# Performance work log

Hardware: AMD Instinct MI355X
Metric: run time of the kernel (lower is better)

## Reference

```python
import jax, jax.numpy as jnp
import numpy as np

B, C, H, W = 4, 256, 224, 224
WH = WW = 8
SH = SW = 4
HEADS = 8
HD = C // HEADS
N = WH * WW
EPS = 1e-5


def _rel_index():
    coords = np.stack(np.meshgrid(np.arange(WH), np.arange(WW), indexing='ij')).reshape(2, -1)
    rel = (coords[:, :, None] - coords[:, None, :]).transpose(1, 2, 0).copy()
    rel[:, :, 0] += WH - 1
    rel[:, :, 1] += WW - 1
    rel[:, :, 0] *= 2 * WW - 1
    return rel.sum(-1)  # (N, N) int

REL_INDEX = _rel_index()


def _shift_mask(Hp, Wp):
    # Swin shift mask for one image: (nW, N, N) float, 0 or -100
    img = np.zeros((Hp, Wp))
    cnt = 0
    for a, b in [(0, Hp - WH), (Hp - WH, Hp - SH), (Hp - SH, Hp)]:
        for c, d in [(0, Wp - WW), (Wp - WW, Wp - SW), (Wp - SW, Wp)]:
            img[a:b, c:d] = cnt
            cnt += 1
    mw = img.reshape(Hp // WH, WH, Wp // WW, WW).transpose(0, 2, 1, 3).reshape(-1, N)
    diff = mw[:, None, :] - mw[:, :, None]  # [w, i, j] = mw[w,j] - mw[w,i]
    return np.where(diff != 0, np.float32(-100.0), np.float32(0.0)).astype(np.float32)


def _ln(x, w, b):
    m = jnp.mean(x, axis=-1, keepdims=True)
    v = jnp.mean(jnp.square(x - m), axis=-1, keepdims=True)
    return (x - m) * jax.lax.rsqrt(v + EPS) * w + b


def setup_inputs() -> dict:
    key = jax.random.key(0)
    ks = jax.random.split(key, 8)
    num_rel = (2 * WH - 1) * (2 * WW - 1)
    return {
        'x': jax.random.normal(ks[0], (B, C, H, W), dtype=jnp.float32),
        'qkv_w': jax.random.normal(ks[1], (3 * C, C), dtype=jnp.float32) * 0.02,
        'proj_w': jax.random.normal(ks[2], (C, C), dtype=jnp.float32) * 0.02,
        'proj_b': jnp.zeros((C,), dtype=jnp.float32),
        'rpb_table': jax.random.normal(ks[3], (num_rel, HEADS), dtype=jnp.float32) * 0.02,
        'norm1_w': jnp.ones((C,), dtype=jnp.float32),
        'norm1_b': jnp.zeros((C,), dtype=jnp.float32),
        'norm2_w': jnp.ones((C,), dtype=jnp.float32),
        'norm2_b': jnp.zeros((C,), dtype=jnp.float32),
        'mlp_w1': jax.random.normal(ks[4], (4 * C, C), dtype=jnp.float32) * 0.02,
        'mlp_b1': jnp.zeros((4 * C,), dtype=jnp.float32),
        'mlp_w2': jax.random.normal(ks[5], (C, 4 * C), dtype=jnp.float32) * 0.02,
        'mlp_b2': jnp.zeros((C,), dtype=jnp.float32),
    }


def reference(x, qkv_w, proj_w, proj_b, rpb_table, norm1_w, norm1_b,
              norm2_w, norm2_b, mlp_w1, mlp_b1, mlp_w2, mlp_b2):
    Bx, Cx, Hx, Wx = x.shape
    pad_h = (WH - Hx % WH) % WH
    pad_w = (WW - Wx % WW) % WW
    if pad_h or pad_w:
        x = jnp.pad(x, ((0, 0), (0, 0), (0, pad_h), (0, pad_w)))
    Hp, Wp = Hx + pad_h, Wx + pad_w
    x = jnp.transpose(x, (0, 2, 3, 1))                    # BHWC
    x = jnp.roll(x, (-SH, -SW), axis=(1, 2))
    nW = (Hp // WH) * (Wp // WW)
    # window partition -> (B*nW, N, C), batch-major
    xw = x.reshape(Bx, Hp // WH, WH, Wp // WW, WW, Cx)
    xw = jnp.transpose(xw, (0, 1, 3, 2, 4, 5)).reshape(-1, N, Cx)

    # ----- windowed attention -----
    h = _ln(xw, norm1_w, norm1_b)
    qkv = (h @ qkv_w.T).reshape(-1, N, 3, HEADS, HD)
    qkv = jnp.transpose(qkv, (2, 0, 3, 1, 4))             # (3, Bw, heads, N, hd)
    q, k, v = qkv[0], qkv[1], qkv[2]
    attn = jnp.einsum('bhnd,bhmd->bhnm', q, k) * (1.0 / HD ** 0.5)
    bias = jnp.transpose(rpb_table[REL_INDEX.reshape(-1)].reshape(N, N, HEADS), (2, 0, 1))
    attn = attn + bias[None]
    # faithful to torch: repeat_interleave(B, dim=0) -> window-major mask ordering
    mask = jnp.asarray(_shift_mask(Hp, Wp))               # (nW, N, N)
    attn = attn + jnp.repeat(mask, Bx, axis=0)[:, None]
    attn = jax.nn.softmax(attn, axis=-1)
    out = jnp.einsum('bhnm,bhmd->bhnd', attn, v)
    out = jnp.transpose(out, (0, 2, 1, 3)).reshape(-1, N, Cx)
    out = out @ proj_w.T + proj_b
    xw = xw + out

    # ----- MLP -----
    h = _ln(xw, norm2_w, norm2_b)
    h = jax.nn.gelu(h @ mlp_w1.T + mlp_b1, approximate=False) @ mlp_w2.T + mlp_b2
    xw = xw + h

    # window reverse, un-shift, un-pad
    x = xw.reshape(Bx, Hp // WH, Wp // WW, WH, WW, Cx)
    x = jnp.transpose(x, (0, 1, 3, 2, 4, 5)).reshape(Bx, Hp, Wp, Cx)
    x = jnp.roll(x, (SH, SW), axis=(1, 2))
    x = x[:, :Hx, :Wx, :]
    return jnp.transpose(x, (0, 3, 1, 2))
```

## Files before the change

### kernel.cpp

```cpp
#include <hip/hip_runtime.h>

typedef unsigned short u16;
typedef unsigned int   u32;
typedef __attribute__((ext_vector_type(8))) __bf16 bf16x8;
typedef __attribute__((ext_vector_type(4))) float  f32x4;
typedef __attribute__((ext_vector_type(4))) u16    u16x4;
typedef __attribute__((ext_vector_type(8))) u16    u16x8;

#define DEV __device__ __forceinline__

DEV u16 f2b(float f) {
  union { float f; u32 u; } a; a.f = f;
  const u32 u = a.u;
  return (u16)((u + 0x7fffu + ((u >> 16) & 1u)) >> 16);
}

DEV float gelu_fast(float x) {
  const float x2 = x * x;
  const float t  = __builtin_fmaf(0.1029430f, x2, 2.3022150f);
  const float e  = __builtin_exp2f(x * t);
  const float r  = __builtin_amdgcn_rcpf(1.0f + e);
  return __builtin_fmaf(-x, r, x);
}

DEV void gload16(const void* g, void* l) {
  __builtin_amdgcn_global_load_lds(
      (const __attribute__((address_space(1))) void*)g,
      (__attribute__((address_space(3))) void*)l, 16, 0, 0);
}

__global__ __launch_bounds__(256)
void conv_weights(const float* __restrict__ qkvw, const float* __restrict__ projw,
                  const float* __restrict__ w1,   const float* __restrict__ w2,
                  u16* __restrict__ dq, u16* __restrict__ dp,
                  u16* __restrict__ d1, u16* __restrict__ d2) {
  const int t = blockIdx.x * 256 + threadIdx.x;
  if (t < 196608)      dq[t]          = f2b(qkvw[t]);
  else if (t < 262144) dp[t - 196608] = f2b(projw[t - 196608]);
  else if (t < 524288) d1[t - 262144] = f2b(w1[t - 262144]);
  else                 d2[t - 524288] = f2b(w2[t - 524288]);
}

__global__ __launch_bounds__(256)
void ln1_win(const float* __restrict__ x, const float* __restrict__ w1,
             const float* __restrict__ b1, u16* __restrict__ hout,
             float* __restrict__ xwout) {
  __shared__ float xt[64 * 257];
  __shared__ float smean[256], srstd[256];
  const int tid = threadIdx.x, lane = tid & 63, wv = tid >> 6;
  const int g = blockIdx.x;
  const int b = g / 196, rem = g % 196;
  const int wh = rem / 7, wg = rem % 7;
  const int base_r = b * 784 + wh * 28 + wg * 4;
  const int pr = tid >> 5, pc = tid & 31;
  int hp = wh * 8 + 4 + pr; if (hp >= 224) hp -= 224;
  int wp = wg * 32 + 4 + pc; if (wp >= 224) wp -= 224;
  const long roff = (long)b * 256 * 50176 + hp * 224 + wp;

  float s = 0.f, q = 0.f;
  for (int cc = 0; cc < 4; ++cc) {
#pragma unroll 8
    for (int i = 0; i < 64; ++i) {
      const int c = cc * 64 + i;
      const float v = x[(long)c * 50176 + roff];
      xt[i * 257 + tid] = v;
      s += v; q += v * v;
    }
    __syncthreads();
#pragma unroll 8
    for (int jj = 0; jj < 64; ++jj) {
      const int p = jj * 4 + wv;
      const int m = (base_r + ((p & 31) >> 3)) * 64 + (p >> 5) * 8 + (p & 7);
      xwout[(long)m * 256 + cc * 64 + lane] = xt[lane * 257 + p];
    }
    __syncthreads();
  }
  const float mean = s * (1.f / 256.f);
  smean[tid] = mean;
  srstd[tid] = rsqrtf(q * (1.f / 256.f) - mean * mean + 1e-5f);
  __syncthreads();

  float wr_[4], br_[4];
#pragma unroll
  for (int cc = 0; cc < 4; ++cc) { wr_[cc] = w1[cc * 64 + lane]; br_[cc] = b1[cc * 64 + lane]; }
#pragma unroll 2
  for (int jj = 0; jj < 64; ++jj) {
    const int p = jj * 4 + wv;
    const int m = (base_r + ((p & 31) >> 3)) * 64 + (p >> 5) * 8 + (p & 7);
    const float mu = smean[p], rs = srstd[p];
#pragma unroll
    for (int cc = 0; cc < 4; ++cc) {
      const float v = xwout[(long)m * 256 + cc * 64 + lane];
      hout[(long)m * 256 + cc * 64 + lane] = f2b((v - mu) * rs * wr_[cc] + br_[cc]);
    }
  }
}

template<int EPI, int NCOL>
__global__ __launch_bounds__(1024, 4)
void gemm_bt(const u16* __restrict__ A, const u16* __restrict__ Bw, const int K,
             float* __restrict__ fout, const float* __restrict__ bias,
             u16* __restrict__ bout,
             const float* __restrict__ lnw, const float* __restrict__ lnb,
             float* __restrict__ oout) {
  __shared__ __align__(16) u16 smem[65536];
  u16* sA0 = smem;
  u16* sB0 = smem + 16384;
  u16* sA1 = smem + 32768;
  u16* sB1 = smem + 49152;

  const int tid  = threadIdx.x;
  const int lane = tid & 63;
  const int wid  = tid >> 6;
  const int wrr  = wid >> 2;
  const int wcc  = wid & 3;

  const int nwg = gridDim.x;
  const int bid = blockIdx.x;
  const int wg  = (bid & 7) * (nwg >> 3) + (bid >> 3);
  const int row_blk = wg / NCOL;
  const int col_blk = wg - row_blk * NCOL;
  const int row0 = row_blk * 256;
  const int col0 = col_blk * 256;

  const f32x4 vzero = {0.f, 0.f, 0.f, 0.f};
  f32x4 acc[4][4];
#pragma unroll
  for (int i = 0; i < 4; ++i)
#pragma unroll
    for (int j = 0; j < 4; ++j) acc[i][j] = vzero;

  const int lrow = lane >> 3;
  const int lcol = ((lane & 7) << 3) ^ (lane & 56);
  const int l15  = lane & 15;
  const int l4   = lane >> 4;
  const int ksw  = (lane & 7) << 3;

  const u16* pA = A  + (long)(row0 + wid * 8 + lrow) * K + lcol;
  const u16* pB = Bw + (long)(col0 + wid * 8 + lrow) * K + lcol;

#define STAGE_TILE(KT, DA, DB)                                          \
  {                                                                     \
    _Pragma("unroll")                                                   \
    for (int ch = 0; ch < 2; ++ch) {                                    \
      gload16(pA + (long)(ch * 128) * K + (KT), (DA) + (ch * 128 + wid * 8) * 64); \
      gload16(pB + (long)(ch * 128) * K + (KT), (DB) + (ch * 128 + wid * 8) * 64); \
    }                                                                   \
  }

#define COMPUTE_TILE(SA, SB, SWAP)                                                      \
  {                                                                                     \
    _Pragma("unroll")                                                                   \
    for (int kk = 0; kk < 2; ++kk) {                                                    \
      bf16x8 af[4], bfv[4];                                                             \
      _Pragma("unroll")                                                                 \
      for (int mi = 0; mi < 4; ++mi)                                                    \
        af[mi] = *(const bf16x8*)((SA) + (wrr * 64 + mi * 16 + l15) * 64 +              \
                                  ((kk * 32 + l4 * 8) ^ ksw));                          \
      _Pragma("unroll")                                                                 \
      for (int nj = 0; nj < 4; ++nj)                                                    \
        bfv[nj] = *(const bf16x8*)((SB) + (wcc * 64 + nj * 16 + l15) * 64 +             \
                                   ((kk * 32 + l4 * 8) ^ ksw));                         \
      _Pragma("unroll")                                                                 \
      for (int mi = 0; mi < 4; ++mi)                                                    \
        _Pragma("unroll")                                                               \
        for (int nj = 0; nj < 4; ++nj) {                                                \
          if (SWAP)                                                                     \
            acc[mi][nj] = __builtin_amdgcn_mfma_f32_16x16x32_bf16(bfv[nj], af[mi],      \
                                                                  acc[mi][nj], 0, 0, 0);\
          else                                                                          \
            acc[mi][nj] = __builtin_amdgcn_mfma_f32_16x16x32_bf16(af[mi], bfv[nj],      \
                                                                  acc[mi][nj], 0, 0, 0);\
        }                                                                               \
    }                                                                                   \
  }

#define KLOOP(SWAP)                                                  \
  {                                                                  \
    const int nt = K >> 6;                                           \
    STAGE_TILE(0, sA0, sB0);                                         \
    int cur = 0;                                                     \
    for (int t = 0; t < nt; ++t) {                                   \
      u16* cA = cur ? sA1 : sA0;                                     \
      u16* cB = cur ? sB1 : sB0;                                     \
      u16* nA = cur ? sA0 : sA1;                                     \
      u16* nB = cur ? sB0 : sB1;                                     \
      if (t + 1 < nt) {                                              \
        STAGE_TILE((t + 1) << 6, nA, nB);                            \
        asm volatile("s_waitcnt vmcnt(4)" ::: "memory");             \
      } else {                                                       \
        asm volatile("s_waitcnt vmcnt(0)" ::: "memory");             \
      }                                                              \
      __builtin_amdgcn_s_barrier();                                  \
      asm volatile("" ::: "memory");                                 \
      COMPUTE_TILE(cA, cB, SWAP);                                    \
      asm volatile("" ::: "memory");                                 \
      __builtin_amdgcn_s_barrier();                                  \
      cur ^= 1;                                                      \
    }                                                                \
  }

  if (EPI == 0 && col_blk == 2) {
    KLOOP(0);
#pragma unroll
    for (int mi = 0; mi < 4; ++mi) {
      const int mb = row0 + wrr * 64 + mi * 16 + (l4 << 2);
      const int rrg = mb >> 6, ii = mb & 63;
#pragma unroll
      for (int nj = 0; nj < 4; ++nj) {
        const int n = 512 + wcc * 64 + nj * 16 + l15;
        const int hh = (n >> 5) & 7, d = n & 31;
        u16x4 p;
#pragma unroll
        for (int reg = 0; reg < 4; ++reg) p[reg] = f2b(acc[mi][nj][reg]);
        *(u16x4*)(bout + 102760448L + (long)((rrg * 8 + hh) * 32 + d) * 64 + ii) = p;
      }
    }
    return;
  }

  KLOOP(1);

#undef STAGE_TILE
#undef COMPUTE_TILE
#undef KLOOP

  if (EPI == 0) {
#pragma unroll
    for (int mi = 0; mi < 4; ++mi) {
      const int m = row0 + wrr * 64 + mi * 16 + l15;
      const int rr = m >> 6, ii = m & 63;
#pragma unroll
      for (int nj = 0; nj < 4; ++nj) {
        const int n = col0 + wcc * 64 + nj * 16 + (l4 << 2);
        const int s = n >> 8, hh = (n >> 5) & 7, d = n & 31;
        u16x4 p;
#pragma unroll
        for (int reg = 0; reg < 4; ++reg) p[reg] = f2b(acc[mi][nj][reg]);
        *(u16x4*)(bout + (long)s * 51380224L +
                  (long)((rr * 8 + hh) * 64 + ii) * 32 + d) = p;
      }
    }
  } else if (EPI == 1) {
    f32x4 b4[4];
#pragma unroll
    for (int nj = 0; nj < 4; ++nj)
      b4[nj] = *(const f32x4*)(bias + wcc * 64 + nj * 16 + (l4 << 2));
    float sS[4], sQ[4];
#pragma unroll
    for (int mi = 0; mi < 4; ++mi) {
      const int m = row0 + wrr * 64 + mi * 16 + l15;
      float* yrow = fout + (long)m * 256;
      float s = 0.f, q = 0.f;
#pragma unroll
      for (int nj = 0; nj < 4; ++nj) {
        const int n = wcc * 64 + nj * 16 + (l4 << 2);
        f32x4 o = *(f32x4*)(yrow + n);
#pragma unroll
        for (int reg = 0; reg < 4; ++reg) {
          o[reg] += acc[mi][nj][reg] + b4[nj][reg];
          s += o[reg]; q += o[reg] * o[reg];
        }
        *(f32x4*)(yrow + n) = o;
        acc[mi][nj] = o;
      }
      s += __shfl_xor(s, 16); s += __shfl_xor(s, 32);
      q += __shfl_xor(q, 16); q += __shfl_xor(q, 32);
      sS[mi] = s; sQ[mi] = q;
    }
    float* ps = (float*)smem;
    float* pq = ps + 1024;
    __syncthreads();
    if (lane < 16) {
#pragma unroll
      for (int mi = 0; mi < 4; ++mi) {
        const int idx = ((wrr * 4 + mi) * 16 + l15) * 4 + wcc;
        ps[idx] = sS[mi]; pq[idx] = sQ[mi];
      }
    }
    __syncthreads();
#pragma unroll
    for (int mi = 0; mi < 4; ++mi) {
      const int m = row0 + wrr * 64 + mi * 16 + l15;
      const int base = ((wrr * 4 + mi) * 16 + l15) * 4;
      const float S = ps[base] + ps[base + 1] + ps[base + 2] + ps[base + 3];
      const float Q = pq[base] + pq[base + 1] + pq[base + 2] + pq[base + 3];
      const float mean = S * (1.f / 256.f);
      const float rstd = rsqrtf(Q * (1.f / 256.f) - mean * mean + 1e-5f);
#pragma unroll
      for (int nj = 0; nj < 4; ++nj) {
        const int n = wcc * 64 + nj * 16 + (l4 << 2);
        const f32x4 w4 = *(const f32x4*)(lnw + n);
        const f32x4 c4 = *(const f32x4*)(lnb + n);
        u16x4 p;
#pragma unroll
        for (int reg = 0; reg < 4; ++reg)
          p[reg] = f2b((acc[mi][nj][reg] - mean) * rstd * w4[reg] + c4[reg]);
        *(u16x4*)(bout + (long)m * 256 + n) = p;
      }
    }
  } else if (EPI == 3) {
    f32x4 b4[4];
#pragma unroll
    for (int nj = 0; nj < 4; ++nj)
      b4[nj] = *(const f32x4*)(bias + wcc * 64 + nj * 16 + (l4 << 2));
#pragma unroll
    for (int mi = 0; mi < 4; ++mi) {
      const int m = row0 + wrr * 64 + mi * 16 + l15;
      const float* yrow = fout + (long)m * 256;
#pragma unroll
      for (int nj = 0; nj < 4; ++nj) {
        const int n = wcc * 64 + nj * 16 + (l4 << 2);
        const f32x4 yv = *(const f32x4*)(yrow + n);
#pragma unroll
        for (int reg = 0; reg < 4; ++reg)
          acc[mi][nj][reg] += yv[reg] + b4[nj][reg];
      }
    }
    const int g = row0 >> 8;
    const int b = g / 196, rem = g % 196;
    const int wh = rem / 7, wg2 = rem % 7;
    float* tp = (float*)smem;
    const int pidx = tid & 255, cgrp = tid >> 8;
    const int pr = pidx >> 5, pc = pidx & 31;
    int hp = wh * 8 + 4 + pr; if (hp >= 224) hp -= 224;
    int wp = wg2 * 32 + 4 + pc; if (wp >= 224) wp -= 224;
    float* ob = oout + (long)b * 256 * 50176 + hp * 224 + wp;
    const int pxr = 4 * (pr * 8 + (pc & 7)) + (pc >> 3);
#pragma unroll
    for (int cc = 0; cc < 4; ++cc) {
      __syncthreads();
      if (wcc == cc) {
#pragma unroll
        for (int mi = 0; mi < 4; ++mi) {
          const int pxw = (4 * (mi * 16 + l15) + wrr) ^ l4;
#pragma unroll
          for (int nj = 0; nj < 4; ++nj)
#pragma unroll
            for (int reg = 0; reg < 4; ++reg)
              tp[(nj * 16 + (l4 << 2) + reg) * 256 + pxw] = acc[mi][nj][reg];
        }
      }
      __syncthreads();
#pragma unroll 4
      for (int j = 0; j < 16; ++j) {
        const int c_local = cgrp * 16 + j;
        ob[(long)(cc * 64 + c_local) * 50176] =
            tp[c_local * 256 + (pxr ^ ((j >> 2) & 3))];
      }
    }
  } else if (EPI == 2) {
    f32x4 b4[4];
#pragma unroll
    for (int nj = 0; nj < 4; ++nj)
      b4[nj] = *(const f32x4*)(bias + col0 + wcc * 64 + nj * 16 + (l4 << 2));
#pragma unroll
    for (int mi = 0; mi < 4; ++mi) {
      const int m = row0 + wrr * 64 + mi * 16 + l15;
#pragma unroll
      for (int nj = 0; nj < 4; ++nj) {
        const int n = col0 + wcc * 64 + nj * 16 + (l4 << 2);
        u16x4 p;
#pragma unroll
        for (int reg = 0; reg < 4; ++reg)
          p[reg] = f2b(gelu_fast(acc[mi][nj][reg] + b4[nj][reg]));
        *(u16x4*)(bout + (long)m * 1024 + n) = p;
      }
    }
  }
}

__global__ __launch_bounds__(256)
void attn_win(const u16* __restrict__ qkv, const float* __restrict__ rpb,
              u16* __restrict__ aout) {
  __shared__ u16 Pl[4][4096];
  __shared__ float srpb[1800];
  const int tid = threadIdx.x, lane = tid & 63, wv = tid >> 6;
  const int bid = blockIdx.x;
  const int r = bid >> 1;
  const int h = (bid & 1) * 4 + wv;
  for (int i = tid; i < 1800; i += 256) srpb[i] = rpb[i];
  __syncthreads();

  const int midx = r >> 2;
  const int wh = midx / 28, ww = midx % 28;
  const int l15 = lane & 15, l4 = lane >> 4;

  u16* Pw = &Pl[wv][0];
  const long hb = (long)(r * 8 + h) * 2048;
  const u16* qh = qkv + hb;
  const u16* kh = qkv + 51380224 + hb;
  const u16* vh = qkv + 102760448 + hb;

  int rj[4], cj[4], labj[4];
#pragma unroll
  for (int nj = 0; nj < 4; ++nj) {
    const int j = nj * 16 + l15;
    rj[nj] = j >> 3; cj[nj] = j & 7;
    const int hp = wh * 8 + rj[nj], wp = ww * 8 + cj[nj];
    const int lh = (hp < 216) ? 0 : ((hp < 220) ? 1 : 2);
    const int lw = (wp < 216) ? 0 : ((wp < 220) ? 1 : 2);
    labj[nj] = lh * 3 + lw;
  }

  const f32x4 vzero = {0.f, 0.f, 0.f, 0.f};

  bf16x8 qf[4], kf[4];
#pragma unroll
  for (int mi = 0; mi < 4; ++mi)
    qf[mi] = *(const bf16x8*)(qh + (mi * 16 + l15) * 32 + l4 * 8);
#pragma unroll
  for (int nj = 0; nj < 4; ++nj)
    kf[nj] = *(const bf16x8*)(kh + (nj * 16 + l15) * 32 + l4 * 8);

  f32x4 S[4][4];
#pragma unroll
  for (int mi = 0; mi < 4; ++mi)
#pragma unroll
    for (int nj = 0; nj < 4; ++nj)
      S[mi][nj] = __builtin_amdgcn_mfma_f32_16x16x32_bf16(qf[mi], kf[nj], vzero, 0, 0, 0);

#pragma unroll
  for (int mi = 0; mi < 4; ++mi)
#pragma unroll
    for (int reg = 0; reg < 4; ++reg) {
      const int i = mi * 16 + (l4 << 2) + reg;
      const int ri = i >> 3, ci = i & 7;
      const int hp = wh * 8 + ri, wp = ww * 8 + ci;
      const int lh = (hp < 216) ? 0 : ((hp < 220) ? 1 : 2);
      const int lw = (wp < 216) ? 0 : ((wp < 220) ? 1 : 2);
      const int li = lh * 3 + lw;
      float v[4];
#pragma unroll
      for (int nj = 0; nj < 4; ++nj) {
        const int idx = (ri - rj[nj] + 7) * 15 + (ci - cj[nj] + 7);
        v[nj] = S[mi][nj][reg] * 0.17677669529663687f + srpb[idx * 8 + h]
              + ((li != labj[nj]) ? -100.0f : 0.0f);
      }
      float mx = fmaxf(fmaxf(v[0], v[1]), fmaxf(v[2], v[3]));
      mx = fmaxf(mx, __shfl_xor(mx, 1));
      mx = fmaxf(mx, __shfl_xor(mx, 2));
      mx = fmaxf(mx, __shfl_xor(mx, 4));
      mx = fmaxf(mx, __shfl_xor(mx, 8));
      float sum = 0.f;
#pragma unroll
      for (int nj = 0; nj < 4; ++nj) { v[nj] = __expf(v[nj] - mx); sum += v[nj]; }
      sum += __shfl_xor(sum, 1);
      sum += __shfl_xor(sum, 2);
      sum += __shfl_xor(sum, 4);
      sum += __shfl_xor(sum, 8);
      const float rinv = __builtin_amdgcn_rcpf(sum);
      const int sw = (i & 7) << 3;
#pragma unroll
      for (int nj = 0; nj < 4; ++nj)
        Pw[i * 64 + ((nj * 16 + l15) ^ sw)] = f2b(v[nj] * rinv);
    }

  f32x4 OT[2][4];
#pragma unroll
  for (int td = 0; td < 2; ++td)
#pragma unroll
    for (int ti = 0; ti < 4; ++ti) OT[td][ti] = vzero;

  const int rsw = (l15 & 7) << 3;
#pragma unroll
  for (int kk = 0; kk < 2; ++kk) {
    bf16x8 pf[4], vf[2];
#pragma unroll
    for (int ti = 0; ti < 4; ++ti)
      pf[ti] = *(const bf16x8*)(Pw + (ti * 16 + l15) * 64 + ((kk * 32 + l4 * 8) ^ rsw));
#pragma unroll
    for (int td = 0; td < 2; ++td)
      vf[td] = *(const bf16x8*)(vh + (td * 16 + l15) * 64 + kk * 32 + l4 * 8);
#pragma unroll
    for (int td = 0; td < 2; ++td)
#pragma unroll
      for (int ti = 0; ti < 4; ++ti)
        OT[td][ti] = __builtin_amdgcn_mfma_f32_16x16x32_bf16(vf[td], pf[ti], OT[td][ti], 0, 0, 0);
  }

#pragma unroll
  for (int td = 0; td < 2; ++td)
#pragma unroll
    for (int ti = 0; ti < 4; ++ti) {
      const int i = ti * 16 + l15;
      const int d0 = td * 16 + (l4 << 2);
      u16x4 p;
#pragma unroll
      for (int reg = 0; reg < 4; ++reg) p[reg] = f2b(OT[td][ti][reg]);
      *(u16x4*)(aout + (long)(r * 64 + i) * 256 + h * 32 + d0) = p;
    }
}

extern "C" void kernel_launch(void* const* d_in, const int* in_sizes, int n_in,
                              void* d_out, int out_size, void* d_ws, size_t ws_size,
                              hipStream_t stream) {
  (void)in_sizes; (void)n_in; (void)out_size; (void)ws_size;
  const float* x     = (const float*)d_in[0];
  const float* qkvw  = (const float*)d_in[1];
  const float* projw = (const float*)d_in[2];
  const float* projb = (const float*)d_in[3];
  const float* rpb   = (const float*)d_in[4];
  const float* n1w   = (const float*)d_in[5];
  const float* n1b   = (const float*)d_in[6];
  const float* n2w   = (const float*)d_in[7];
  const float* n2b   = (const float*)d_in[8];
  const float* w1    = (const float*)d_in[9];
  const float* b1    = (const float*)d_in[10];
  const float* w2    = (const float*)d_in[11];
  const float* b2    = (const float*)d_in[12];

  char* ws = (char*)d_ws;
  u16*   hbuf   = (u16*)(ws);
  u16*   qkvb   = (u16*)(ws + 102760448);
  u16*   abuf   = (u16*)(ws + 411041792);
  float* ybuf   = (float*)(ws + 513802240);
  u16*   hidb   = (u16*)(ws + 102760448);
  u16*   qkvwb  = (u16*)(ws + 719323136);
  u16*   projwb = (u16*)(ws + 719716352);
  u16*   w1b    = (u16*)(ws + 719847424);
  u16*   w2b    = (u16*)(ws + 720371712);

  conv_weights<<<3072, 256, 0, stream>>>(qkvw, projw, w1, w2, qkvwb, projwb, w1b, w2b);
  ln1_win<<<784, 256, 0, stream>>>(x, n1w, n1b, hbuf, ybuf);
  gemm_bt<0, 3><<<2352, 1024, 0, stream>>>(hbuf, qkvwb, 256, nullptr, nullptr, qkvb, nullptr, nullptr, nullptr);
  attn_win<<<6272, 256, 0, stream>>>(qkvb, rpb, abuf);
  gemm_bt<1, 1><<<784, 1024, 0, stream>>>(abuf, projwb, 256, ybuf, projb, hbuf, n2w, n2b, nullptr);
  gemm_bt<2, 4><<<3136, 1024, 0, stream>>>(hbuf, w1b, 256, nullptr, b1, hidb, nullptr, nullptr, nullptr);
  gemm_bt<3, 1><<<784, 1024, 0, stream>>>(hidb, w2b, 1024, ybuf, b2, nullptr, nullptr, nullptr, (float*)d_out);
}
```

Baseline: 1.125 ms.

## Shrink GEMM tile to 128x256 with 8 waves and BK=32 staging

Changes the bf16 GEMM from 1024-thread 256x256 tiles with a K-step of 64 to 512-thread 128x256 tiles with a K-step of 32. This cuts LDS use from 128KB to 48KB so more blocks can be resident per CU and the grid doubles. The staging swizzle, LDS fragment loads, LN reduction indexing and the un-window transpose epilogue are rewritten to match. The trade-off is less B-operand reuse per tile and twice as many barriers per K, in exchange for higher occupancy and better load balance.

```diff
diff --git a/kernel.cpp b/kernel.cpp
--- a/kernel.cpp
+++ b/kernel.cpp
@@ -97,17 +97,17 @@
 }
 
 template<int EPI, int NCOL>
-__global__ __launch_bounds__(1024, 4)
+__global__ __launch_bounds__(512, 4)
 void gemm_bt(const u16* __restrict__ A, const u16* __restrict__ Bw, const int K,
              float* __restrict__ fout, const float* __restrict__ bias,
              u16* __restrict__ bout,
              const float* __restrict__ lnw, const float* __restrict__ lnb,
              float* __restrict__ oout) {
-  __shared__ __align__(16) u16 smem[65536];
+  __shared__ __align__(16) u16 smem[24576];
   u16* sA0 = smem;
-  u16* sB0 = smem + 16384;
-  u16* sA1 = smem + 32768;
-  u16* sB1 = smem + 49152;
+  u16* sB0 = smem + 4096;
+  u16* sA1 = smem + 12288;
+  u16* sB1 = smem + 16384;
 
   const int tid  = threadIdx.x;
   const int lane = tid & 63;
@@ -120,7 +120,7 @@
   const int wg  = (bid & 7) * (nwg >> 3) + (bid >> 3);
   const int row_blk = wg / NCOL;
   const int col_blk = wg - row_blk * NCOL;
-  const int row0 = row_blk * 256;
+  const int row0 = row_blk * 128;
   const int col0 = col_blk * 256;
 
   const f32x4 vzero = {0.f, 0.f, 0.f, 0.f};
@@ -130,54 +130,50 @@
 #pragma unroll
     for (int j = 0; j < 4; ++j) acc[i][j] = vzero;
 
-  const int lrow = lane >> 3;
-  const int lcol = ((lane & 7) << 3) ^ (lane & 56);
   const int l15  = lane & 15;
   const int l4   = lane >> 4;
-  const int ksw  = (lane & 7) << 3;
-
-  const u16* pA = A  + (long)(row0 + wid * 8 + lrow) * K + lcol;
-  const u16* pB = Bw + (long)(col0 + wid * 8 + lrow) * K + lcol;
-
-#define STAGE_TILE(KT, DA, DB)                                          \
-  {                                                                     \
-    _Pragma("unroll")                                                   \
-    for (int ch = 0; ch < 2; ++ch) {                                    \
-      gload16(pA + (long)(ch * 128) * K + (KT), (DA) + (ch * 128 + wid * 8) * 64); \
-      gload16(pB + (long)(ch * 128) * K + (KT), (DB) + (ch * 128 + wid * 8) * 64); \
-    }                                                                   \
+  const int ksw2 = (l15 >> 1) & 3;
+  const int lcol = (((tid & 3) ^ ((tid >> 3) & 3)) << 3);
+
+  const u16* pA  = A  + (long)(row0 + (tid >> 2)) * K + lcol;
+  const u16* pB  = Bw + (long)(col0 + (tid >> 2)) * K + lcol;
+  const u16* pB2 = pB + (long)128 * K;
+  const int wbase = wid * 512;
+
+#define STAGE_TILE(KT, DA, DB)                  \
+  {                                             \
+    gload16(pA  + (KT), (DA) + wbase);          \
+    gload16(pB  + (KT), (DB) + wbase);          \
+    gload16(pB2 + (KT), (DB) + 4096 + wbase);   \
   }
 
 #define COMPUTE_TILE(SA, SB, SWAP)                                                      \
   {                                                                                     \
+    bf16x8 af[4], bfv[4];                                                               \
     _Pragma("unroll")                                                                   \
-    for (int kk = 0; kk < 2; ++kk) {                                                    \
-      bf16x8 af[4], bfv[4];                                                             \
+    for (int mi = 0; mi < 4; ++mi)                                                      \
+      af[mi] = *(const bf16x8*)((SA) + (wrr * 64 + mi * 16 + l15) * 32 +                \
+                                ((l4 ^ ksw2) << 3));                                    \
+    _Pragma("unroll")                                                                   \
+    for (int nj = 0; nj < 4; ++nj)                                                      \
+      bfv[nj] = *(const bf16x8*)((SB) + (wcc * 64 + nj * 16 + l15) * 32 +               \
+                                 ((l4 ^ ksw2) << 3));                                   \
+    _Pragma("unroll")                                                                   \
+    for (int mi = 0; mi < 4; ++mi)                                                      \
       _Pragma("unroll")                                                                 \
-      for (int mi = 0; mi < 4; ++mi)                                                    \
-        af[mi] = *(const bf16x8*)((SA) + (wrr * 64 + mi * 16 + l15) * 64 +              \
-                                  ((kk * 32 + l4 * 8) ^ ksw));                          \
-      _Pragma("unroll")                                                                 \
-      for (int nj = 0; nj < 4; ++nj)                                                    \
-        bfv[nj] = *(const bf16x8*)((SB) + (wcc * 64 + nj * 16 + l15) * 64 +             \
-                                   ((kk * 32 + l4 * 8) ^ ksw));                         \
-      _Pragma("unroll")                                                                 \
-      for (int mi = 0; mi < 4; ++mi)                                                    \
-        _Pragma("unroll")                                                               \
-        for (int nj = 0; nj < 4; ++nj) {                                                \
-          if (SWAP)                                                                     \
-            acc[mi][nj] = __builtin_amdgcn_mfma_f32_16x16x32_bf16(bfv[nj], af[mi],      \
-                                                                  acc[mi][nj], 0, 0, 0);\
-          else                                                                          \
-            acc[mi][nj] = __builtin_amdgcn_mfma_f32_16x16x32_bf16(af[mi], bfv[nj],      \
-                                                                  acc[mi][nj], 0, 0, 0);\
-        }                                                                               \
-    }                                                                                   \
+      for (int nj = 0; nj < 4; ++nj) {                                                  \
+        if (SWAP)                                                                       \
+          acc[mi][nj] = __builtin_amdgcn_mfma_f32_16x16x32_bf16(bfv[nj], af[mi],        \
+                                                                acc[mi][nj], 0, 0, 0);  \
+        else                                                                            \
+          acc[mi][nj] = __builtin_amdgcn_mfma_f32_16x16x32_bf16(af[mi], bfv[nj],        \
+                                                                acc[mi][nj], 0, 0, 0);  \
+      }                                                                                 \
   }
 
 #define KLOOP(SWAP)                                                  \
   {                                                                  \
-    const int nt = K >> 6;                                           \
+    const int nt = K >> 5;                                           \
     STAGE_TILE(0, sA0, sB0);                                         \
     int cur = 0;                                                     \
     for (int t = 0; t < nt; ++t) {                                   \
@@ -186,8 +182,8 @@
       u16* nA = cur ? sA0 : sA1;                                     \
       u16* nB = cur ? sB0 : sB1;                                     \
       if (t + 1 < nt) {                                              \
-        STAGE_TILE((t + 1) << 6, nA, nB);                            \
-        asm volatile("s_waitcnt vmcnt(4)" ::: "memory");             \
+        STAGE_TILE((t + 1) << 5, nA, nB);                            \
+        asm volatile("s_waitcnt vmcnt(3)" ::: "memory");             \
       } else {                                                       \
         asm volatile("s_waitcnt vmcnt(0)" ::: "memory");             \
       }                                                              \
@@ -269,12 +265,12 @@
       sS[mi] = s; sQ[mi] = q;
     }
     float* ps = (float*)smem;
-    float* pq = ps + 1024;
+    float* pq = ps + 512;
     __syncthreads();
     if (lane < 16) {
 #pragma unroll
       for (int mi = 0; mi < 4; ++mi) {
-        const int idx = ((wrr * 4 + mi) * 16 + l15) * 4 + wcc;
+        const int idx = (wrr * 64 + mi * 16 + l15) * 4 + wcc;
         ps[idx] = sS[mi]; pq[idx] = sQ[mi];
       }
     }
@@ -282,7 +278,7 @@
 #pragma unroll
     for (int mi = 0; mi < 4; ++mi) {
       const int m = row0 + wrr * 64 + mi * 16 + l15;
-      const int base = ((wrr * 4 + mi) * 16 + l15) * 4;
+      const int base = (wrr * 64 + mi * 16 + l15) * 4;
       const float S = ps[base] + ps[base + 1] + ps[base + 2] + ps[base + 3];
       const float Q = pq[base] + pq[base + 1] + pq[base + 2] + pq[base + 3];
       const float mean = S * (1.f / 256.f);
@@ -317,36 +313,37 @@
           acc[mi][nj][reg] += yv[reg] + b4[nj][reg];
       }
     }
-    const int g = row0 >> 8;
-    const int b = g / 196, rem = g % 196;
-    const int wh = rem / 7, wg2 = rem % 7;
+    const int wr0 = row0 >> 6;
+    const int b = wr0 / 784, rem = wr0 % 784;
+    const int wh = rem / 28, wwb = rem % 28;
     float* tp = (float*)smem;
-    const int pidx = tid & 255, cgrp = tid >> 8;
-    const int pr = pidx >> 5, pc = pidx & 31;
-    int hp = wh * 8 + 4 + pr; if (hp >= 224) hp -= 224;
-    int wp = wg2 * 32 + 4 + pc; if (wp >= 224) wp -= 224;
+    const int pidx = tid & 127, cgrp = tid >> 7;
+    const int pr = pidx >> 4, pc = pidx & 15;
+    int hp = wh * 8 + 4 + pr;  if (hp >= 224) hp -= 224;
+    int wp = wwb * 8 + 4 + pc; if (wp >= 224) wp -= 224;
     float* ob = oout + (long)b * 256 * 50176 + hp * 224 + wp;
-    const int pxr = 4 * (pr * 8 + (pc & 7)) + (pc >> 3);
 #pragma unroll
     for (int cc = 0; cc < 4; ++cc) {
       __syncthreads();
       if (wcc == cc) {
 #pragma unroll
         for (int mi = 0; mi < 4; ++mi) {
-          const int pxw = (4 * (mi * 16 + l15) + wrr) ^ l4;
+          const int ml = wrr * 64 + mi * 16 + l15;
+          const int px = ((ml & 63) >> 3) * 16 + (ml >> 6) * 8 + (ml & 7);
 #pragma unroll
           for (int nj = 0; nj < 4; ++nj)
 #pragma unroll
             for (int reg = 0; reg < 4; ++reg)
-              tp[(nj * 16 + (l4 << 2) + reg) * 256 + pxw] = acc[mi][nj][reg];
+              tp[(nj * 16 + (l4 << 2) + reg) * 128 + (px ^ (l4 << 2))] =
+                  acc[mi][nj][reg];
         }
       }
       __syncthreads();
 #pragma unroll 4
       for (int j = 0; j < 16; ++j) {
-        const int c_local = cgrp * 16 + j;
-        ob[(long)(cc * 64 + c_local) * 50176] =
-            tp[c_local * 256 + (pxr ^ ((j >> 2) & 3))];
+        const int cl = cgrp * 16 + j;
+        ob[(long)(cc * 64 + cl) * 50176] =
+            tp[cl * 128 + (pidx ^ (((cl >> 2) & 3) << 2))];
       }
     }
   } else if (EPI == 2) {
@@ -523,9 +520,9 @@
 
   conv_weights<<<3072, 256, 0, stream>>>(qkvw, projw, w1, w2, qkvwb, projwb, w1b, w2b);
   ln1_win<<<784, 256, 0, stream>>>(x, n1w, n1b, hbuf, ybuf);
-  gemm_bt<0, 3><<<2352, 1024, 0, stream>>>(hbuf, qkvwb, 256, nullptr, nullptr, qkvb, nullptr, nullptr, nullptr);
+  gemm_bt<0, 3><<<4704, 512, 0, stream>>>(hbuf, qkvwb, 256, nullptr, nullptr, qkvb, nullptr, nullptr, nullptr);
   attn_win<<<6272, 256, 0, stream>>>(qkvb, rpb, abuf);
-  gemm_bt<1, 1><<<784, 1024, 0, stream>>>(abuf, projwb, 256, ybuf, projb, hbuf, n2w, n2b, nullptr);
-  gemm_bt<2, 4><<<3136, 1024, 0, stream>>>(hbuf, w1b, 256, nullptr, b1, hidb, nullptr, nullptr, nullptr);
-  gemm_bt<3, 1><<<784, 1024, 0, stream>>>(hidb, w2b, 1024, ybuf, b2, nullptr, nullptr, nullptr, (float*)d_out);
-}
+  gemm_bt<1, 1><<<1568, 512, 0, stream>>>(abuf, projwb, 256, ybuf, projb, hbuf, n2w, n2b, nullptr);
+  gemm_bt<2, 4><<<6272, 512, 0, stream>>>(hbuf, w1b, 256, nullptr, b1, hidb, nullptr, nullptr, nullptr);
+  gemm_bt<3, 1><<<1568, 512, 0, stream>>>(hidb, w2b, 1024, ybuf, b2, nullptr, nullptr, nullptr, (float*)d_out);
+}
```

After: 1.130 ms. No clear change (+0.5%).
